# Kernel tuning notes

Measured on AMD Instinct MI355X. Metric: run time of the kernel, lower is better.

The kernel has to match this reference:

```python
import jax, jax.numpy as jnp
import numpy as np

TEMPERATURE = 0.1

def setup_inputs() -> dict:
    key = jax.random.key(0)
    k1, k2 = jax.random.split(key)
    B, D, NUM_CLASSES = 4096, 512, 64
    emb = jax.random.normal(k1, (B, D), dtype=jnp.float32)
    # L2-normalize so sims/temperature stays in a safe range for exp()
    emb = emb / jnp.linalg.norm(emb, axis=1, keepdims=True)
    labels = jax.random.randint(k2, (B,), 0, NUM_CLASSES, dtype=jnp.int64)
    return {"embeddings": emb, "labels": labels}

def reference(embeddings, labels):
    B = embeddings.shape[0]
    # [B, B] similarity matrix, scaled by temperature
    sims = jnp.matmul(embeddings, embeddings.T) / TEMPERATURE
    same = labels[:, None] == labels[None, :]
    eye = jnp.eye(B, dtype=bool)
    pos_mask = (same & ~eye).astype(sims.dtype)   # positives, diagonal excluded
    neg_mask = (~same).astype(sims.dtype)          # negatives
    exp_s = jnp.exp(sims)
    # denominator[i] = sum over negatives of exp_s[i, :]
    denom = jnp.sum(exp_s * neg_mask, axis=1, keepdims=True)  # [B, 1]
    # per positive pair (i, j): -log(exp_s[i,j] / (denom[i] + exp_s[i,j]))
    per_pair = -jnp.log(exp_s / (denom + exp_s))
    loss_sum = jnp.sum(per_pair * pos_mask)
    num_pos = jnp.sum(pos_mask)
    return loss_sum / jnp.maximum(num_pos, 1.0)
```

## Files before the change

kernel.cpp:

```cpp
#include <hip/hip_runtime.h>
#include <hip/hip_bf16.h>

#define B_N 4096
#define D_K 512
#define INV_T 10.0f

#define BM 128
#define CPB 128
#define CS 64
#define NCG (CPB / 16)
#define SLOTS 16
#define NTILES 528

typedef __attribute__((ext_vector_type(4))) float float4v;

#define WS_TERS   0
#define WS_CNTF   16384
#define WS_DENOM  32768
#define WS_POSCNT 1081344
#define WS_POSS   2129920
#define WS_EMBF   18907136

__global__ __launch_bounds__(256) void k0_convert(const float* __restrict__ emb,
                                                  unsigned char* __restrict__ embF) {
    int t    = blockIdx.x * 256 + threadIdx.x;
    int kc   = t & 15;
    int lane = (t >> 4) & 63;
    int g    = t >> 10;
    int l16  = lane & 15;
    int quad = lane >> 4;
    int row  = g * 16 + l16;
    int kq   = kc * 4 + quad;
    const float* sp = emb + row * D_K + kq * 8;
    float4 v0 = *(const float4*)(sp);
    float4 v1 = *(const float4*)(sp + 4);
    int lo = __builtin_amdgcn_cvt_pk_fp8_f32(v0.x, v0.y, 0, false);
    lo     = __builtin_amdgcn_cvt_pk_fp8_f32(v0.z, v0.w, lo, true);
    int hi = __builtin_amdgcn_cvt_pk_fp8_f32(v1.x, v1.y, 0, false);
    hi     = __builtin_amdgcn_cvt_pk_fp8_f32(v1.z, v1.w, hi, true);
    int2 o; o.x = lo; o.y = hi;
    *(int2*)(embF + ((size_t)(g * 64 + lane) * 16 + kc) * 8) = o;
}

__global__ __launch_bounds__(256, 2) void k1_denom(const unsigned char* __restrict__ embF,
                                                   const int* __restrict__ labels,
                                                   float* __restrict__ denomPart,
                                                   int* __restrict__ posCnt,
                                                   float* __restrict__ posS) {
    __shared__ float sPos[BM * SLOTS];
    __shared__ int   sCnt[BM];
    __shared__ float sPosC[2 * CPB * SLOTS];
    __shared__ int   sCntC[2 * CPB];
    __shared__ float sColW[4 * CPB];

    const int tid  = threadIdx.x;
    const int wave = tid >> 6;
    const int lane = tid & 63;
    const int quad = lane >> 4;
    const int l16  = lane & 15;

    const int t0 = blockIdx.x;
    int R = 0, accT = 0;
    while (accT + (32 - R) <= t0) { accT += 32 - R; ++R; }
    const int C = R + (t0 - accT);
    const bool isDiag = (C == R);
    const int rowBase = R * BM;

    if (tid < BM) sCnt[tid] = 0;
    sCntC[tid] = 0;
    __syncthreads();

    long afrag[2][16];
#pragma unroll
    for (int t = 0; t < 2; ++t) {
        const int g = R * 8 + wave * 2 + t;
        const unsigned char* ap = embF + (size_t)(g * 64 + lane) * 128;
#pragma unroll
        for (int i = 0; i < 8; ++i) {
            long2 v = *(const long2*)(ap + i * 16);
            afrag[t][2 * i]     = v.x;
            afrag[t][2 * i + 1] = v.y;
        }
    }

    int labI[2][4];
#pragma unroll
    for (int t = 0; t < 2; ++t)
#pragma unroll
        for (int r = 0; r < 4; ++r)
            labI[t][r] = labels[rowBase + wave * 32 + t * 16 + quad * 4 + r];

    int labJ[NCG];
#pragma unroll
    for (int cg = 0; cg < NCG; ++cg)
        labJ[cg] = labels[C * CPB + cg * 16 + l16];

    float rowAcc[2][4] = {{0.f,0.f,0.f,0.f},{0.f,0.f,0.f,0.f}};

#pragma unroll
    for (int cg = 0; cg < NCG; ++cg) {
        const unsigned char* bp = embF + (size_t)((C * NCG + cg) * 64 + lane) * 128;
        long bfrag[16];
#pragma unroll
        for (int i = 0; i < 8; ++i) {
            long2 v = *(const long2*)(bp + i * 16);
            bfrag[2 * i]     = v.x;
            bfrag[2 * i + 1] = v.y;
        }

        float4v acc[2];
        acc[0] = (float4v){0.f, 0.f, 0.f, 0.f};
        acc[1] = (float4v){0.f, 0.f, 0.f, 0.f};
#pragma unroll
        for (int kc = 0; kc < 16; ++kc) {
            acc[0] = __builtin_amdgcn_mfma_f32_16x16x32_fp8_fp8(afrag[0][kc], bfrag[kc], acc[0], 0, 0, 0);
            acc[1] = __builtin_amdgcn_mfma_f32_16x16x32_fp8_fp8(afrag[1][kc], bfrag[kc], acc[1], 0, 0, 0);
        }

        const int col = C * CPB + cg * 16 + l16;
        const int lJ  = labJ[cg];
        float cAcc = 0.0f;
#pragma unroll
        for (int t = 0; t < 2; ++t) {
#pragma unroll
            for (int r = 0; r < 4; ++r) {
                float s = acc[t][r] * INV_T;
                const int lr = wave * 32 + t * 16 + quad * 4 + r;
                if (lJ != labI[t][r]) {
                    float e = __expf(s);
                    rowAcc[t][r] += e;
                    cAcc += e;
                } else if (col != rowBase + lr) {
                    int idx = atomicAdd(&sCnt[lr], 1);
                    if (idx < SLOTS) sPos[lr * SLOTS + idx] = s;
                    if (!isDiag) {
                        int ci = (wave >> 1) * CPB + cg * 16 + l16;
                        int idx2 = atomicAdd(&sCntC[ci], 1);
                        if (idx2 < SLOTS) sPosC[ci * SLOTS + idx2] = s;
                    }
                }
            }
        }
        if (!isDiag) {
            cAcc += __shfl_xor(cAcc, 16);
            cAcc += __shfl_xor(cAcc, 32);
            if (quad == 0) sColW[wave * CPB + cg * 16 + l16] = cAcc;
        }
    }

#pragma unroll
    for (int t = 0; t < 2; ++t)
#pragma unroll
        for (int r = 0; r < 4; ++r) {
            float v = rowAcc[t][r];
            v += __shfl_xor(v, 1);
            v += __shfl_xor(v, 2);
            v += __shfl_xor(v, 4);
            v += __shfl_xor(v, 8);
            if (l16 == 0) {
                const int row = rowBase + wave * 32 + t * 16 + quad * 4 + r;
                denomPart[row * CS + 2 * C]     = v;
                denomPart[row * CS + 2 * C + 1] = 0.0f;
            }
        }

    __syncthreads();

    if (tid < BM) {
        const int row = rowBase + tid;
        const int c   = min(sCnt[tid], SLOTS);
        posCnt[row * CS + 2 * C]     = c;
        posCnt[row * CS + 2 * C + 1] = 0;
        for (int m = 0; m < c; ++m)
            posS[(row * CS + 2 * C) * SLOTS + m] = sPos[tid * SLOTS + m];
    }
    if (!isDiag) {
        const int s0 = tid >> 7;
        const int cc = tid & (CPB - 1);
        const int j  = C * CPB + cc;
        const int sp = 2 * R + s0;
        denomPart[j * CS + sp] = sColW[(2 * s0) * CPB + cc] + sColW[(2 * s0 + 1) * CPB + cc];
        const int ci = s0 * CPB + cc;
        const int c  = min(sCntC[ci], SLOTS);
        posCnt[j * CS + sp] = c;
        for (int m = 0; m < c; ++m)
            posS[(j * CS + sp) * SLOTS + m] = sPosC[ci * SLOTS + m];
    }
}

__global__ __launch_bounds__(256) void k2_pos(const float* __restrict__ denomPart,
                                              const int* __restrict__ posCnt,
                                              const float* __restrict__ posS,
                                              float* __restrict__ termSum,
                                              float* __restrict__ cntF) {
    const int wave = threadIdx.x >> 6;
    const int lane = threadIdx.x & 63;
    const int i    = blockIdx.x * 4 + wave;

    float d  = denomPart[i * CS + lane];
    int   cb = posCnt[i * CS + lane];
    float c  = (float)cb;
#pragma unroll
    for (int off = 32; off; off >>= 1) {
        d += __shfl_xor(d, off);
        c += __shfl_xor(c, off);
    }

    float sum = 0.0f;
    const float* ps = posS + (i * CS + lane) * SLOTS;
    for (int m = 0; m < cb; ++m) {
        float s = ps[m];
        sum += __logf(d + __expf(s)) - s;
    }
#pragma unroll
    for (int off = 32; off; off >>= 1) sum += __shfl_xor(sum, off);
    if (lane == 0) { termSum[i] = sum; cntF[i] = c; }
}

__global__ __launch_bounds__(256) void k3_final(const float* __restrict__ termSum,
                                                const float* __restrict__ cntF,
                                                float* __restrict__ out) {
    __shared__ float sL[256], sC[256];
    float ls = 0.0f, cs = 0.0f;
    for (int i = threadIdx.x; i < B_N; i += 256) { ls += termSum[i]; cs += cntF[i]; }
    sL[threadIdx.x] = ls; sC[threadIdx.x] = cs;
    __syncthreads();
    for (int s = 128; s; s >>= 1) {
        if (threadIdx.x < s) {
            sL[threadIdx.x] += sL[threadIdx.x + s];
            sC[threadIdx.x] += sC[threadIdx.x + s];
        }
        __syncthreads();
    }
    if (threadIdx.x == 0) out[0] = sL[0] / fmaxf(sC[0], 1.0f);
}

extern "C" void kernel_launch(void* const* d_in, const int* in_sizes, int n_in,
                              void* d_out, int out_size, void* d_ws, size_t ws_size,
                              hipStream_t stream) {
    const float* emb    = (const float*)d_in[0];
    const int*   labels = (const int*)d_in[1];
    float*       out    = (float*)d_out;

    char* ws = (char*)d_ws;
    float*         termSum   = (float*)(ws + WS_TERS);
    float*         cntF      = (float*)(ws + WS_CNTF);
    float*         denomPart = (float*)(ws + WS_DENOM);
    int*           posCnt    = (int*)(ws + WS_POSCNT);
    float*         posS      = (float*)(ws + WS_POSS);
    unsigned char* embF      = (unsigned char*)(ws + WS_EMBF);

    k0_convert<<<dim3(B_N * D_K / 8 / 256), dim3(256), 0, stream>>>(emb, embF);

    k1_denom<<<dim3(NTILES), dim3(256), 0, stream>>>(embF, labels, denomPart, posCnt, posS);

    k2_pos<<<dim3(B_N / 4), dim3(256), 0, stream>>>(denomPart, posCnt, posS, termSum, cntF);

    k3_final<<<dim3(1), dim3(256), 0, stream>>>(termSum, cntF, out);
}
```

Before: 112.8 us.

## Shrink symmetric tiles to 64x64 for more blocks and higher occupancy

Cuts the upper-triangular similarity tile from 128x128 to 64x64, which raises the tile count from 528 to 2080 so more blocks can spread across the GPU. Each wave now holds one A fragment instead of two, and launch bounds ask for 4 blocks per CU. Labels are staged once in shared memory, and inline asm pins the fragment registers so the loads are not rematerialised. Column partials are now written one slot per row tile, with no paired zero slot. The cost is less reuse per B fragment load, more redundant B traffic and more per-tile overhead.

```diff
diff --git a/kernel.cpp b/kernel.cpp
--- a/kernel.cpp
+++ b/kernel.cpp
@@ -5,14 +5,19 @@
 #define D_K 512
 #define INV_T 10.0f
 
-#define BM 128
-#define CPB 128
+#define BM 64
+#define CPB 64
 #define CS 64
 #define NCG (CPB / 16)
 #define SLOTS 16
-#define NTILES 528
+#define NTILES 2080
 
 typedef __attribute__((ext_vector_type(4))) float float4v;
+typedef __attribute__((ext_vector_type(2))) long lx2;
+
+#define KEEP8(a0,a1,a2,a3,a4,a5,a6,a7)                                     \
+    asm volatile("" : "+v"(a0), "+v"(a1), "+v"(a2), "+v"(a3),              \
+                      "+v"(a4), "+v"(a5), "+v"(a6), "+v"(a7))
 
 #define WS_TERS   0
 #define WS_CNTF   16384
@@ -42,16 +47,17 @@
     *(int2*)(embF + ((size_t)(g * 64 + lane) * 16 + kc) * 8) = o;
 }
 
-__global__ __launch_bounds__(256, 2) void k1_denom(const unsigned char* __restrict__ embF,
+__global__ __launch_bounds__(256, 4) void k1_denom(const unsigned char* __restrict__ embF,
                                                    const int* __restrict__ labels,
                                                    float* __restrict__ denomPart,
                                                    int* __restrict__ posCnt,
                                                    float* __restrict__ posS) {
     __shared__ float sPos[BM * SLOTS];
     __shared__ int   sCnt[BM];
-    __shared__ float sPosC[2 * CPB * SLOTS];
-    __shared__ int   sCntC[2 * CPB];
+    __shared__ float sPosC[CPB * SLOTS];
+    __shared__ int   sCntC[CPB];
     __shared__ float sColW[4 * CPB];
+    __shared__ int   sLab[BM + CPB];
 
     const int tid  = threadIdx.x;
     const int wave = tid >> 6;
@@ -60,84 +66,85 @@
     const int l16  = lane & 15;
 
     const int t0 = blockIdx.x;
-    int R = 0, accT = 0;
-    while (accT + (32 - R) <= t0) { accT += 32 - R; ++R; }
-    const int C = R + (t0 - accT);
+    int R = 0;
+    while ((R + 1) * (129 - (R + 1)) / 2 <= t0) ++R;
+    const int C = R + (t0 - R * (129 - R) / 2);
     const bool isDiag = (C == R);
     const int rowBase = R * BM;
 
-    if (tid < BM) sCnt[tid] = 0;
-    sCntC[tid] = 0;
+    long afrag[16];
+    {
+        const int g = R * 4 + wave;
+        const unsigned char* ap = embF + (size_t)(g * 64 + lane) * 128;
+#pragma unroll
+        for (int i = 0; i < 8; ++i) {
+            lx2 v = *(const lx2*)(ap + i * 16);
+            afrag[2 * i]     = v[0];
+            afrag[2 * i + 1] = v[1];
+        }
+    }
+
+    if (tid < BM)                   { sCnt[tid] = 0; sLab[tid] = labels[rowBase + tid]; }
+    else if (tid < BM + CPB)        { sCntC[tid - BM] = 0; sLab[tid] = labels[C * CPB + (tid - BM)]; }
     __syncthreads();
 
-    long afrag[2][16];
-#pragma unroll
-    for (int t = 0; t < 2; ++t) {
-        const int g = R * 8 + wave * 2 + t;
-        const unsigned char* ap = embF + (size_t)(g * 64 + lane) * 128;
-#pragma unroll
-        for (int i = 0; i < 8; ++i) {
-            long2 v = *(const long2*)(ap + i * 16);
-            afrag[t][2 * i]     = v.x;
-            afrag[t][2 * i + 1] = v.y;
-        }
-    }
-
-    int labI[2][4];
-#pragma unroll
-    for (int t = 0; t < 2; ++t)
-#pragma unroll
-        for (int r = 0; r < 4; ++r)
-            labI[t][r] = labels[rowBase + wave * 32 + t * 16 + quad * 4 + r];
+    KEEP8(afrag[0], afrag[1], afrag[2],  afrag[3],
+          afrag[4], afrag[5], afrag[6],  afrag[7]);
+    KEEP8(afrag[8], afrag[9], afrag[10], afrag[11],
+          afrag[12], afrag[13], afrag[14], afrag[15]);
+
+    int labI[4];
+#pragma unroll
+    for (int r = 0; r < 4; ++r)
+        labI[r] = sLab[wave * 16 + quad * 4 + r];
 
     int labJ[NCG];
 #pragma unroll
     for (int cg = 0; cg < NCG; ++cg)
-        labJ[cg] = labels[C * CPB + cg * 16 + l16];
-
-    float rowAcc[2][4] = {{0.f,0.f,0.f,0.f},{0.f,0.f,0.f,0.f}};
+        labJ[cg] = sLab[BM + cg * 16 + l16];
+
+    float rowAcc[4] = {0.f, 0.f, 0.f, 0.f};
 
 #pragma unroll
     for (int cg = 0; cg < NCG; ++cg) {
-        const unsigned char* bp = embF + (size_t)((C * NCG + cg) * 64 + lane) * 128;
         long bfrag[16];
-#pragma unroll
-        for (int i = 0; i < 8; ++i) {
-            long2 v = *(const long2*)(bp + i * 16);
-            bfrag[2 * i]     = v.x;
-            bfrag[2 * i + 1] = v.y;
-        }
-
-        float4v acc[2];
-        acc[0] = (float4v){0.f, 0.f, 0.f, 0.f};
-        acc[1] = (float4v){0.f, 0.f, 0.f, 0.f};
-#pragma unroll
-        for (int kc = 0; kc < 16; ++kc) {
-            acc[0] = __builtin_amdgcn_mfma_f32_16x16x32_fp8_fp8(afrag[0][kc], bfrag[kc], acc[0], 0, 0, 0);
-            acc[1] = __builtin_amdgcn_mfma_f32_16x16x32_fp8_fp8(afrag[1][kc], bfrag[kc], acc[1], 0, 0, 0);
-        }
+        {
+            const unsigned char* bp = embF + (size_t)((C * NCG + cg) * 64 + lane) * 128;
+#pragma unroll
+            for (int i = 0; i < 8; ++i) {
+                lx2 v = *(const lx2*)(bp + i * 16);
+                bfrag[2 * i]     = v[0];
+                bfrag[2 * i + 1] = v[1];
+            }
+        }
+        KEEP8(bfrag[0], bfrag[1], bfrag[2],  bfrag[3],
+              bfrag[4], bfrag[5], bfrag[6],  bfrag[7]);
+        KEEP8(bfrag[8], bfrag[9], bfrag[10], bfrag[11],
+              bfrag[12], bfrag[13], bfrag[14], bfrag[15]);
+
+        float4v acc = (float4v){0.f, 0.f, 0.f, 0.f};
+#pragma unroll
+        for (int kc = 0; kc < 16; ++kc)
+            acc = __builtin_amdgcn_mfma_f32_16x16x32_fp8_fp8(afrag[kc], bfrag[kc], acc, 0, 0, 0);
 
         const int col = C * CPB + cg * 16 + l16;
         const int lJ  = labJ[cg];
         float cAcc = 0.0f;
 #pragma unroll
-        for (int t = 0; t < 2; ++t) {
-#pragma unroll
-            for (int r = 0; r < 4; ++r) {
-                float s = acc[t][r] * INV_T;
-                const int lr = wave * 32 + t * 16 + quad * 4 + r;
-                if (lJ != labI[t][r]) {
-                    float e = __expf(s);
-                    rowAcc[t][r] += e;
-                    cAcc += e;
-                } else if (col != rowBase + lr) {
-                    int idx = atomicAdd(&sCnt[lr], 1);
-                    if (idx < SLOTS) sPos[lr * SLOTS + idx] = s;
-                    if (!isDiag) {
-                        int ci = (wave >> 1) * CPB + cg * 16 + l16;
-                        int idx2 = atomicAdd(&sCntC[ci], 1);
-                        if (idx2 < SLOTS) sPosC[ci * SLOTS + idx2] = s;
-                    }
+        for (int r = 0; r < 4; ++r) {
+            float s = acc[r] * INV_T;
+            const int lr = wave * 16 + quad * 4 + r;
+            if (lJ != labI[r]) {
+                float e = __expf(s);
+                rowAcc[r] += e;
+                cAcc += e;
+            } else if (col != rowBase + lr) {
+                int idx = atomicAdd(&sCnt[lr], 1);
+                if (idx < SLOTS) sPos[lr * SLOTS + idx] = s;
+                if (!isDiag) {
+                    int ci = cg * 16 + l16;
+                    int idx2 = atomicAdd(&sCntC[ci], 1);
+                    if (idx2 < SLOTS) sPosC[ci * SLOTS + idx2] = s;
                 }
             }
         }
@@ -149,42 +156,34 @@
     }
 
 #pragma unroll
-    for (int t = 0; t < 2; ++t)
-#pragma unroll
-        for (int r = 0; r < 4; ++r) {
-            float v = rowAcc[t][r];
-            v += __shfl_xor(v, 1);
-            v += __shfl_xor(v, 2);
-            v += __shfl_xor(v, 4);
-            v += __shfl_xor(v, 8);
-            if (l16 == 0) {
-                const int row = rowBase + wave * 32 + t * 16 + quad * 4 + r;
-                denomPart[row * CS + 2 * C]     = v;
-                denomPart[row * CS + 2 * C + 1] = 0.0f;
-            }
-        }
+    for (int r = 0; r < 4; ++r) {
+        float v = rowAcc[r];
+        v += __shfl_xor(v, 1);
+        v += __shfl_xor(v, 2);
+        v += __shfl_xor(v, 4);
+        v += __shfl_xor(v, 8);
+        if (l16 == 0)
+            denomPart[(rowBase + wave * 16 + quad * 4 + r) * CS + C] = v;
+    }
 
     __syncthreads();
 
     if (tid < BM) {
         const int row = rowBase + tid;
         const int c   = min(sCnt[tid], SLOTS);
-        posCnt[row * CS + 2 * C]     = c;
-        posCnt[row * CS + 2 * C + 1] = 0;
+        posCnt[row * CS + C] = c;
         for (int m = 0; m < c; ++m)
-            posS[(row * CS + 2 * C) * SLOTS + m] = sPos[tid * SLOTS + m];
-    }
-    if (!isDiag) {
-        const int s0 = tid >> 7;
-        const int cc = tid & (CPB - 1);
+            posS[(row * CS + C) * SLOTS + m] = sPos[tid * SLOTS + m];
+    }
+    if (!isDiag && tid >= 128 && tid < 128 + CPB) {
+        const int cc = tid - 128;
         const int j  = C * CPB + cc;
-        const int sp = 2 * R + s0;
-        denomPart[j * CS + sp] = sColW[(2 * s0) * CPB + cc] + sColW[(2 * s0 + 1) * CPB + cc];
-        const int ci = s0 * CPB + cc;
-        const int c  = min(sCntC[ci], SLOTS);
-        posCnt[j * CS + sp] = c;
+        denomPart[j * CS + R] = sColW[0 * CPB + cc] + sColW[1 * CPB + cc] +
+                                sColW[2 * CPB + cc] + sColW[3 * CPB + cc];
+        const int c = min(sCntC[cc], SLOTS);
+        posCnt[j * CS + R] = c;
         for (int m = 0; m < c; ++m)
-            posS[(j * CS + sp) * SLOTS + m] = sPosC[ci * SLOTS + m];
+            posS[(j * CS + R) * SLOTS + m] = sPosC[cc * SLOTS + m];
     }
 }
 
```

After: 122.5 us. 1.09x slower.
